# Kernel optimization log

Hardware: AMD Instinct MI355X
Metric: run time of the kernel (lower is better)

The kernel has to match this reference:

```python
import jax, jax.numpy as jnp
import numpy as np

DIM = 1024
HEADS = 16
N_SENTS = 64
N_ENTS = 16
BATCH = 32


def setup_inputs() -> dict:
    key = jax.random.key(0)
    ks = jax.random.split(key, 16)
    S, E, B, D = N_SENTS, N_ENTS, BATCH, DIM
    sc = 1.0 / np.sqrt(D)
    f32 = jnp.float32
    return {
        "entities": jax.random.normal(ks[0], (S * E, B, D), f32),
        "padding_mask": jnp.zeros((S * E, B), bool),
        "n_sents": S,
        # learned aggregation query, init uniform(-1, 1) as in the module
        "query": jax.random.uniform(ks[1], (1, 1, D), f32, -1.0, 1.0),
        # do_proj key/val Linear layers (torch Linear convention: y = x @ W.T + b)
        "Wk_lin": jax.random.normal(ks[2], (D, D), f32) * sc,
        "bk_lin": jnp.zeros((D,), f32),
        "Wv_lin": jax.random.normal(ks[3], (D, D), f32) * sc,
        "bv_lin": jnp.zeros((D,), f32),
        # MultiheadAttention in-projection (split q/k/v) and out-projection
        "Wq_in": jax.random.normal(ks[4], (D, D), f32) * sc,
        "bq_in": jnp.zeros((D,), f32),
        "Wk_in": jax.random.normal(ks[5], (D, D), f32) * sc,
        "bk_in": jnp.zeros((D,), f32),
        "Wv_in": jax.random.normal(ks[6], (D, D), f32) * sc,
        "bv_in": jnp.zeros((D,), f32),
        "Wo": jax.random.normal(ks[7], (D, D), f32) * sc,
        "bo": jnp.zeros((D,), f32),
    }


def reference(entities, padding_mask, n_sents, query,
              Wk_lin, bk_lin, Wv_lin, bv_lin,
              Wq_in, bq_in, Wk_in, bk_in, Wv_in, bv_in, Wo, bo):
    SE, B, D = entities.shape
    E = SE // n_sents
    H = HEADS
    hd = D // H

    # do_proj key/value linears
    keys = entities @ Wk_lin.T + bk_lin   # [SE, B, D]
    vals = entities @ Wv_lin.T + bv_lin   # [SE, B, D]

    # MHA in-projections. Query is a single learned vector shared across
    # sentences and batch, so project once: [H, hd], pre-scaled by 1/sqrt(hd).
    q = ((query[0, 0] @ Wq_in.T + bq_in).reshape(H, hd)) * (1.0 / np.sqrt(hd))
    # Honor the block-diagonal mask: query s only sees its n_ents key slice,
    # so reshape keys/vals to [S, E, B, H, hd] and never build [S, S*E] scores.
    k = (keys @ Wk_in.T + bk_in).reshape(n_sents, E, B, H, hd)
    v = (vals @ Wv_in.T + bv_in).reshape(n_sents, E, B, H, hd)

    scores = jnp.einsum('hd,sebhd->sbhe', q, k)            # [S, B, H, E]
    pm = padding_mask.reshape(n_sents, E, B).transpose(0, 2, 1)  # [S, B, E]
    scores = jnp.where(pm[:, :, None, :], -jnp.inf, scores)
    attn = jax.nn.softmax(scores, axis=-1)                 # [S, B, H, E]
    ctx = jnp.einsum('sbhe,sebhd->sbhd', attn, v).reshape(n_sents, B, D)
    return ctx @ Wo.T + bo                                  # [S, B, D]
```

## Files before the change

### kernel.cpp

```cpp
#include <hip/hip_runtime.h>
#include <hip/hip_bf16.h>

constexpr int kD  = 1024;
constexpr int kH  = 16;
constexpr int kHD = 64;
constexpr int kS  = 64;
constexpr int kE  = 16;
constexpr int kB  = 32;
constexpr int kSB = kS * kB;

typedef __attribute__((ext_vector_type(8))) short bfvec8;
typedef __attribute__((ext_vector_type(4))) float fvec4;

struct __align__(8)  bf4  { __hip_bfloat16 v[4]; };
struct __align__(16) bf8v { __hip_bfloat16 v[8]; };


__global__ __launch_bounds__(256) void k_pre(const float* __restrict__ Wq_in,
                                             const float* __restrict__ query,
                                             const float* __restrict__ bq_in,
                                             const float* __restrict__ Wv_in,
                                             const float* __restrict__ bv_lin,
                                             const float* __restrict__ bv_in,
                                             float* __restrict__ qs,
                                             float* __restrict__ cb,
                                             float* __restrict__ cvec) {
  int j = blockIdx.x, t = threadIdx.x;
  if (j == 0 && t < 16) cvec[t] = 0.f;
  const float *W, *vec, *bias;
  float scale;
  float* outp;
  int row;
  if (j < 1024) { W = Wq_in; vec = query;  bias = bq_in; scale = 0.125f; outp = qs; row = j; }
  else          { W = Wv_in; vec = bv_lin; bias = bv_in; scale = 1.0f;   outp = cb; row = j - 1024; }
  const float4* w4 = (const float4*)(W + (size_t)row * kD);
  const float4* v4 = (const float4*)vec;
  float4 a = w4[t], b = v4[t];
  float acc = a.x * b.x + a.y * b.y + a.z * b.z + a.w * b.w;
  #pragma unroll
  for (int o = 32; o >= 1; o >>= 1) acc += __shfl_xor(acc, o);
  __shared__ float red[4];
  if ((t & 63) == 0) red[t >> 6] = acc;
  __syncthreads();
  if (t == 0) outp[row] = (red[0] + red[1] + red[2] + red[3] + bias[row]) * scale;
}

__global__ __launch_bounds__(256) void k_w2(const float* __restrict__ qs,
                                            const float* __restrict__ Wk_in,
                                            const float* __restrict__ bk_lin,
                                            const float* __restrict__ bk_in,
                                            float* __restrict__ wmat,
                                            float* __restrict__ cvec) {
  int tid = blockIdx.x * 256 + threadIdx.x;
  int h = tid >> 10, d = tid & (kD - 1);
  float acc = 0.f;
  #pragma unroll 8
  for (int j = 0; j < kHD; j++)
    acc = fmaf(qs[h * kHD + j], Wk_in[(size_t)(h * kHD + j) * kD + d], acc);
  wmat[(size_t)h * kD + d] = acc;
  float val = acc * bk_lin[d];
  if (d < kHD) val += qs[h * kHD + d] * bk_in[h * kHD + d];
  #pragma unroll
  for (int o = 32; o >= 1; o >>= 1) val += __shfl_xor(val, o);
  if ((threadIdx.x & 63) == 0) atomicAdd(&cvec[h], val);
}

__global__ __launch_bounds__(256) void k_cvt(const float* __restrict__ in,
                                             __hip_bfloat16* __restrict__ out) {
  int i = (blockIdx.x * 256 + threadIdx.x) * 4;
  float4 v = *(const float4*)(in + i);
  bf4 o;
  o.v[0] = __float2bfloat16(v.x); o.v[1] = __float2bfloat16(v.y);
  o.v[2] = __float2bfloat16(v.z); o.v[3] = __float2bfloat16(v.w);
  *(bf4*)(out + i) = o;
}


__global__ __launch_bounds__(256) void k_attn_eagg(const float* __restrict__ ent,
                                                   const unsigned char* __restrict__ pmask,
                                                   const __hip_bfloat16* __restrict__ Ubf,
                                                   const float* __restrict__ cvec,
                                                   __hip_bfloat16* __restrict__ eagg) {
  __shared__ __hip_bfloat16 ent_s[kE][kD + 8];
  __shared__ float sred[4][kE][kH + 1];
  __shared__ __hip_bfloat16 attn_b[kH][32];
  int sb = blockIdx.x;
  int s = sb >> 5, b = sb & 31;
  int t = threadIdx.x, l = t & 63, w = t >> 6;
  int quad = l >> 4, lane16 = l & 15;

  const float* src = ent + (size_t)(s * kE) * kB * kD + (size_t)b * kD;
  #pragma unroll
  for (int it = 0; it < 8; it++) {
    int i = t + it * 256;
    int e = i >> 7, f = (i & 127) * 8;
    const float4* pp = (const float4*)(src + (size_t)e * kB * kD + f);
    float4 v0 = pp[0], v1 = pp[1];
    bf8v pk;
    pk.v[0] = __float2bfloat16(v0.x); pk.v[1] = __float2bfloat16(v0.y);
    pk.v[2] = __float2bfloat16(v0.z); pk.v[3] = __float2bfloat16(v0.w);
    pk.v[4] = __float2bfloat16(v1.x); pk.v[5] = __float2bfloat16(v1.y);
    pk.v[6] = __float2bfloat16(v1.z); pk.v[7] = __float2bfloat16(v1.w);
    *(bf8v*)&ent_s[e][f] = pk;
  }
  __syncthreads();

  fvec4 sacc = {};
  #pragma unroll
  for (int ks = 0; ks < 8; ks++) {
    int k0 = w * 256 + ks * 32 + quad * 8;
    bfvec8 a = *(const bfvec8*)&ent_s[lane16][k0];
    bfvec8 bb = *(const bfvec8*)&Ubf[(size_t)lane16 * kD + k0];
    sacc = __builtin_amdgcn_mfma_f32_16x16x32_bf16(a, bb, sacc, 0, 0, 0);
  }
  #pragma unroll
  for (int i = 0; i < 4; i++) sred[w][quad * 4 + i][lane16] = sacc[i];
  __syncthreads();

  {
    int h = t >> 4, e = t & 15;
    float sc = sred[0][e][h] + sred[1][e][h] + sred[2][e][h] + sred[3][e][h] + cvec[h];
    if (pmask[(size_t)(s * kE + e) * kB + b]) sc = -INFINITY;
    float m = sc;
    #pragma unroll
    for (int o = 8; o >= 1; o >>= 1) m = fmaxf(m, __shfl_xor(m, o, 16));
    float ex = __expf(sc - m);
    float sum = ex;
    #pragma unroll
    for (int o = 8; o >= 1; o >>= 1) sum += __shfl_xor(sum, o, 16);
    attn_b[h][e] = __float2bfloat16(ex / sum);
    attn_b[h][e + 16] = __float2bfloat16(0.f);
  }
  __syncthreads();

  bfvec8 bfrag = *(const bfvec8*)&attn_b[lane16][quad * 8];
  __hip_bfloat16* dst = eagg + (size_t)sb * (kH * kD);
  for (int tt = 0; tt < 16; tt++) {
    int dme = (w * 16 + tt) * 16 + lane16;
    bfvec8 afrag = {};
    if (quad < 2) {
      #pragma unroll
      for (int j = 0; j < 8; j++)
        afrag[j] = *(const short*)&ent_s[quad * 8 + j][dme];
    }
    fvec4 acc = {};
    acc = __builtin_amdgcn_mfma_f32_16x16x32_bf16(afrag, bfrag, acc, 0, 0, 0);
    int d0 = (w * 16 + tt) * 16 + quad * 4;
    bf4 o;
    o.v[0] = __float2bfloat16(acc[0]); o.v[1] = __float2bfloat16(acc[1]);
    o.v[2] = __float2bfloat16(acc[2]); o.v[3] = __float2bfloat16(acc[3]);
    *(bf4*)&dst[(size_t)lane16 * kD + d0] = o;
  }
}


__device__ __forceinline__ void stage_row(const __hip_bfloat16* g, __hip_bfloat16* s) {
  *(bf8v*)s = *(const bf8v*)g;
}
__device__ __forceinline__ void stage_row(const float* g, __hip_bfloat16* s) {
  const float4* p = (const float4*)g;
  float4 v0 = p[0], v1 = p[1];
  bf8v pk;
  pk.v[0] = __float2bfloat16(v0.x); pk.v[1] = __float2bfloat16(v0.y);
  pk.v[2] = __float2bfloat16(v0.z); pk.v[3] = __float2bfloat16(v0.w);
  pk.v[4] = __float2bfloat16(v1.x); pk.v[5] = __float2bfloat16(v1.y);
  pk.v[6] = __float2bfloat16(v1.z); pk.v[7] = __float2bfloat16(v1.w);
  *(bf8v*)s = pk;
}


template <int MODE, typename TA, typename TB, typename TC>
__global__ __launch_bounds__(256) void k_gemm_mfma(
    const TA* __restrict__ Abase, int lda, long aBatch,
    const TB* __restrict__ Bbase, int ldb, long bBatch,
    TC* __restrict__ Cbase, int ldc, long cBatch,
    const float* __restrict__ bias, long biasBatch, int Ksz) {
  const TA* Ag = Abase + (size_t)blockIdx.z * aBatch;
  const TB* Bg = Bbase + (size_t)blockIdx.z * bBatch;
  TC* Cg = Cbase + (size_t)blockIdx.z * cBatch;
  const float* biasp = bias ? bias + (size_t)blockIdx.z * biasBatch : nullptr;
  const int m0 = blockIdx.x * 64, n0 = blockIdx.y * 64;
  __shared__ __hip_bfloat16 As[64][72];
  __shared__ __hip_bfloat16 Bs[64][72];
  const int t = threadIdx.x;
  const int l = t & 63, w = t >> 6;
  const int quad = l >> 4, col = l & 15;
  fvec4 acc[4] = {};
  for (int k0 = 0; k0 < Ksz; k0 += 64) {
    #pragma unroll
    for (int c = t; c < 512; c += 256) {
      int row = c >> 3, kq = (c & 7) * 8;
      stage_row(Ag + (size_t)(m0 + row) * lda + k0 + kq, &As[row][kq]);
      stage_row(Bg + (size_t)(n0 + row) * ldb + k0 + kq, &Bs[row][kq]);
    }
    __syncthreads();
    #pragma unroll
    for (int ks = 0; ks < 64; ks += 32) {
      bfvec8 a = *(const bfvec8*)&As[w * 16 + col][ks + quad * 8];
      #pragma unroll
      for (int nt = 0; nt < 4; nt++) {
        bfvec8 b = *(const bfvec8*)&Bs[nt * 16 + col][ks + quad * 8];
        acc[nt] = __builtin_amdgcn_mfma_f32_16x16x32_bf16(a, b, acc[nt], 0, 0, 0);
      }
    }
    __syncthreads();
  }
  #pragma unroll
  for (int nt = 0; nt < 4; nt++) {
    int n = n0 + nt * 16 + col;
    float bv = biasp ? biasp[n] : 0.f;
    #pragma unroll
    for (int i = 0; i < 4; i++) {
      int r = m0 + w * 16 + quad * 4 + i;
      float v = acc[nt][i] + bv;
      if constexpr (MODE == 0) ((float*)Cg)[(size_t)r * ldc + n] = v;
      else ((__hip_bfloat16*)Cg)[(size_t)r * ldc + n] = __float2bfloat16(v);
    }
  }
}


__global__ __launch_bounds__(256) void k_gemm_nn(
    const float* __restrict__ Ag, int lda,
    const float* __restrict__ Bg, int ldb,
    __hip_bfloat16* __restrict__ Cg, int ldc, int Ksz) {
  const int m0 = blockIdx.x * 64, n0 = blockIdx.y * 64;
  __shared__ __hip_bfloat16 As[64][72];
  __shared__ __hip_bfloat16 Bs[64][72];
  const int t = threadIdx.x;
  const int l = t & 63, w = t >> 6;
  const int quad = l >> 4, col = l & 15;
  fvec4 acc[4] = {};
  for (int k0 = 0; k0 < Ksz; k0 += 64) {
    #pragma unroll
    for (int c = t; c < 512; c += 256) {
      int row = c >> 3, kq = (c & 7) * 8;
      stage_row(Ag + (size_t)(m0 + row) * lda + k0 + kq, &As[row][kq]);
      const float4* pb = (const float4*)(Bg + (size_t)(k0 + row) * ldb + n0 + kq);
      float4 b0 = pb[0], b1 = pb[1];
      Bs[kq + 0][row] = __float2bfloat16(b0.x);
      Bs[kq + 1][row] = __float2bfloat16(b0.y);
      Bs[kq + 2][row] = __float2bfloat16(b0.z);
      Bs[kq + 3][row] = __float2bfloat16(b0.w);
      Bs[kq + 4][row] = __float2bfloat16(b1.x);
      Bs[kq + 5][row] = __float2bfloat16(b1.y);
      Bs[kq + 6][row] = __float2bfloat16(b1.z);
      Bs[kq + 7][row] = __float2bfloat16(b1.w);
    }
    __syncthreads();
    #pragma unroll
    for (int ks = 0; ks < 64; ks += 32) {
      bfvec8 a = *(const bfvec8*)&As[w * 16 + col][ks + quad * 8];
      #pragma unroll
      for (int nt = 0; nt < 4; nt++) {
        bfvec8 b = *(const bfvec8*)&Bs[nt * 16 + col][ks + quad * 8];
        acc[nt] = __builtin_amdgcn_mfma_f32_16x16x32_bf16(a, b, acc[nt], 0, 0, 0);
      }
    }
    __syncthreads();
  }
  #pragma unroll
  for (int nt = 0; nt < 4; nt++) {
    int n = n0 + nt * 16 + col;
    #pragma unroll
    for (int i = 0; i < 4; i++) {
      int r = m0 + w * 16 + quad * 4 + i;
      Cg[(size_t)r * ldc + n] = __float2bfloat16(acc[nt][i]);
    }
  }
}

extern "C" void kernel_launch(void* const* d_in, const int* in_sizes, int n_in,
                              void* d_out, int out_size, void* d_ws, size_t ws_size,
                              hipStream_t stream) {
  const float* ent            = (const float*)d_in[0];
  const unsigned char* pmask  = (const unsigned char*)d_in[1];
  const float* query          = (const float*)d_in[3];
  const float* Wk_lin         = (const float*)d_in[4];
  const float* bk_lin         = (const float*)d_in[5];
  const float* Wv_lin         = (const float*)d_in[6];
  const float* bv_lin         = (const float*)d_in[7];
  const float* Wq_in          = (const float*)d_in[8];
  const float* bq_in          = (const float*)d_in[9];
  const float* Wk_in          = (const float*)d_in[10];
  const float* bk_in          = (const float*)d_in[11];
  const float* Wv_in          = (const float*)d_in[12];
  const float* bv_in          = (const float*)d_in[13];
  const float* Wo             = (const float*)d_in[14];
  const float* bo             = (const float*)d_in[15];
  float* out = (float*)d_out;

  float* p = (float*)d_ws;
  float* qs   = p; p += 1024;
  float* wmat = p; p += 64 * kD;
  float* cvec = p; p += 256;
  float* cb   = p; p += kD;
  __hip_bfloat16* bp = (__hip_bfloat16*)p;
  __hip_bfloat16* Ubf  = bp; bp += (size_t)64 * kD;
  __hip_bfloat16* Mmat = bp; bp += (size_t)kD * kD;
  __hip_bfloat16* Wobf = bp; bp += (size_t)kD * kD;
  __hip_bfloat16* ctx2 = bp; bp += (size_t)kSB * kD;
  __hip_bfloat16* eagg = bp;

  k_pre<<<2048, 256, 0, stream>>>(Wq_in, query, bq_in, Wv_in, bv_lin, bv_in, qs, cb, cvec);
  k_w2<<<64, 256, 0, stream>>>(qs, Wk_in, bk_lin, bk_in, wmat, cvec);
  k_cvt<<<1024, 256, 0, stream>>>(Wo, Wobf);
  k_gemm_nn<<<dim3(1, 16, 1), 256, 0, stream>>>(wmat, kD, Wk_lin, kD, Ubf, kD, kD);
  k_gemm_nn<<<dim3(16, 16, 1), 256, 0, stream>>>(Wv_in, kD, Wv_lin, kD, Mmat, kD, kD);

  k_attn_eagg<<<kSB, 256, 0, stream>>>(ent, pmask, Ubf, cvec, eagg);
  k_gemm_mfma<2><<<dim3(kSB / 64, 1, kH), 256, 0, stream>>>(
      eagg, kH * kD, (long)kD, Mmat, kD, (long)(kHD * kD),
      ctx2, kD, (long)kHD, cb, (long)kHD, kD);
  k_gemm_mfma<0><<<dim3(kSB / 64, kD / 64, 1), 256, 0, stream>>>(
      ctx2, kD, 0L, Wobf, kD, 0L, out, kD, 0L, bo, 0L, kD);
}
```

Baseline: 354.7 us.

## Double-buffer GEMMs, swizzle workgroups, merge precompute kernels, halve attention MFMA waste

Adds register-prefetch double buffering and workgroup-ID swizzling to both MFMA GEMM kernels, removing one barrier per K step. Folds the Wo conversion and the Wk bias projection into k_pre. It now computes Wk_in·Wk_lin as a full batched GEMM alongside Wv_in·Wv_lin, then forms U from that product in a new small kernel. The attention aggregation kernel uses a cross-lane shuffle so each MFMA carries useful data in both halves rather than zero padding. Together these cut launch count and stall time, but the extra full 1024x1024 GEMM adds precompute work and the product is rounded to bf16 before U is formed.

```diff
diff --git a/kernel.cpp b/kernel.cpp
--- a/kernel.cpp
+++ b/kernel.cpp
@@ -11,10 +11,10 @@
 
 typedef __attribute__((ext_vector_type(8))) short bfvec8;
 typedef __attribute__((ext_vector_type(4))) float fvec4;
+typedef __attribute__((ext_vector_type(4))) int   ivec4;
 
 struct __align__(8)  bf4  { __hip_bfloat16 v[4]; };
 struct __align__(16) bf8v { __hip_bfloat16 v[8]; };
-
 
 __global__ __launch_bounds__(256) void k_pre(const float* __restrict__ Wq_in,
                                              const float* __restrict__ query,
@@ -22,17 +22,31 @@
                                              const float* __restrict__ Wv_in,
                                              const float* __restrict__ bv_lin,
                                              const float* __restrict__ bv_in,
+                                             const float* __restrict__ Wk_in,
+                                             const float* __restrict__ bk_lin,
+                                             const float* __restrict__ bk_in,
+                                             const float* __restrict__ Wo,
                                              float* __restrict__ qs,
                                              float* __restrict__ cb,
-                                             float* __restrict__ cvec) {
+                                             float* __restrict__ kb2,
+                                             __hip_bfloat16* __restrict__ Wobf) {
   int j = blockIdx.x, t = threadIdx.x;
-  if (j == 0 && t < 16) cvec[t] = 0.f;
+  if (j >= 3072) {
+    int i = (j - 3072) * kD + t * 4;
+    float4 v = *(const float4*)(Wo + i);
+    bf4 o;
+    o.v[0] = __float2bfloat16(v.x); o.v[1] = __float2bfloat16(v.y);
+    o.v[2] = __float2bfloat16(v.z); o.v[3] = __float2bfloat16(v.w);
+    *(bf4*)(Wobf + i) = o;
+    return;
+  }
   const float *W, *vec, *bias;
   float scale;
   float* outp;
   int row;
-  if (j < 1024) { W = Wq_in; vec = query;  bias = bq_in; scale = 0.125f; outp = qs; row = j; }
-  else          { W = Wv_in; vec = bv_lin; bias = bv_in; scale = 1.0f;   outp = cb; row = j - 1024; }
+  if (j < 1024)      { W = Wq_in; vec = query;  bias = bq_in; scale = 0.125f; outp = qs;  row = j; }
+  else if (j < 2048) { W = Wv_in; vec = bv_lin; bias = bv_in; scale = 1.0f;   outp = cb;  row = j - 1024; }
+  else               { W = Wk_in; vec = bk_lin; bias = bk_in; scale = 1.0f;   outp = kb2; row = j - 2048; }
   const float4* w4 = (const float4*)(W + (size_t)row * kD);
   const float4* v4 = (const float4*)vec;
   float4 a = w4[t], b = v4[t];
@@ -45,36 +59,35 @@
   if (t == 0) outp[row] = (red[0] + red[1] + red[2] + red[3] + bias[row]) * scale;
 }
 
-__global__ __launch_bounds__(256) void k_w2(const float* __restrict__ qs,
-                                            const float* __restrict__ Wk_in,
-                                            const float* __restrict__ bk_lin,
-                                            const float* __restrict__ bk_in,
-                                            float* __restrict__ wmat,
-                                            float* __restrict__ cvec) {
-  int tid = blockIdx.x * 256 + threadIdx.x;
-  int h = tid >> 10, d = tid & (kD - 1);
+__global__ __launch_bounds__(256) void k_w2p(const float* __restrict__ qs,
+                                             const __hip_bfloat16* __restrict__ KK,
+                                             const float* __restrict__ kb2,
+                                             __hip_bfloat16* __restrict__ Ubf,
+                                             float* __restrict__ cvec) {
+  int bq = blockIdx.x;
+  int h = bq >> 2;
+  int n = (bq & 3) * 256 + threadIdx.x;
   float acc = 0.f;
   #pragma unroll 8
   for (int j = 0; j < kHD; j++)
-    acc = fmaf(qs[h * kHD + j], Wk_in[(size_t)(h * kHD + j) * kD + d], acc);
-  wmat[(size_t)h * kD + d] = acc;
-  float val = acc * bk_lin[d];
-  if (d < kHD) val += qs[h * kHD + d] * bk_in[h * kHD + d];
-  #pragma unroll
-  for (int o = 32; o >= 1; o >>= 1) val += __shfl_xor(val, o);
-  if ((threadIdx.x & 63) == 0) atomicAdd(&cvec[h], val);
-}
-
-__global__ __launch_bounds__(256) void k_cvt(const float* __restrict__ in,
-                                             __hip_bfloat16* __restrict__ out) {
-  int i = (blockIdx.x * 256 + threadIdx.x) * 4;
-  float4 v = *(const float4*)(in + i);
+    acc = fmaf(qs[h * kHD + j], __bfloat162float(KK[(size_t)(h * kHD + j) * kD + n]), acc);
+  Ubf[(size_t)h * kD + n] = __float2bfloat16(acc);
+  if ((bq & 3) == 0 && threadIdx.x < 64) {
+    int t = threadIdx.x;
+    float v = qs[h * kHD + t] * kb2[h * kHD + t];
+    #pragma unroll
+    for (int o = 32; o >= 1; o >>= 1) v += __shfl_xor(v, o);
+    if (t == 0) cvec[h] = v;
+  }
+}
+
+
+__device__ __forceinline__ void st4(__hip_bfloat16* dst, fvec4 a) {
   bf4 o;
-  o.v[0] = __float2bfloat16(v.x); o.v[1] = __float2bfloat16(v.y);
-  o.v[2] = __float2bfloat16(v.z); o.v[3] = __float2bfloat16(v.w);
-  *(bf4*)(out + i) = o;
-}
-
+  o.v[0] = __float2bfloat16(a[0]); o.v[1] = __float2bfloat16(a[1]);
+  o.v[2] = __float2bfloat16(a[2]); o.v[3] = __float2bfloat16(a[3]);
+  *(bf4*)dst = o;
+}
 
 __global__ __launch_bounds__(256) void k_attn_eagg(const float* __restrict__ ent,
                                                    const unsigned char* __restrict__ pmask,
@@ -135,31 +148,31 @@
 
   bfvec8 bfrag = *(const bfvec8*)&attn_b[lane16][quad * 8];
   __hip_bfloat16* dst = eagg + (size_t)sb * (kH * kD);
-  for (int tt = 0; tt < 16; tt++) {
-    int dme = (w * 16 + tt) * 16 + lane16;
-    bfvec8 afrag = {};
-    if (quad < 2) {
-      #pragma unroll
-      for (int j = 0; j < 8; j++)
-        afrag[j] = *(const short*)&ent_s[quad * 8 + j][dme];
-    }
-    fvec4 acc = {};
-    acc = __builtin_amdgcn_mfma_f32_16x16x32_bf16(afrag, bfrag, acc, 0, 0, 0);
-    int d0 = (w * 16 + tt) * 16 + quad * 4;
-    bf4 o;
-    o.v[0] = __float2bfloat16(acc[0]); o.v[1] = __float2bfloat16(acc[1]);
-    o.v[2] = __float2bfloat16(acc[2]); o.v[3] = __float2bfloat16(acc[3]);
-    *(bf4*)&dst[(size_t)lane16 * kD + d0] = o;
-  }
-}
-
-
-__device__ __forceinline__ void stage_row(const __hip_bfloat16* g, __hip_bfloat16* s) {
-  *(bf8v*)s = *(const bf8v*)g;
-}
-__device__ __forceinline__ void stage_row(const float* g, __hip_bfloat16* s) {
-  const float4* p = (const float4*)g;
-  float4 v0 = p[0], v1 = p[1];
+  int eq = (quad & 1) * 8;
+  #pragma unroll
+  for (int tp = 0; tp < 8; tp++) {
+    int tSel = (quad < 2) ? tp : (tp + 8);
+    int dme = (w * 16 + tSel) * 16 + lane16;
+    bfvec8 val;
+    #pragma unroll
+    for (int j = 0; j < 8; j++)
+      val[j] = *(const short*)&ent_s[eq + j][dme];
+    ivec4 vi = __builtin_bit_cast(ivec4, val);
+    ivec4 wi;
+    #pragma unroll
+    for (int r = 0; r < 4; r++) wi[r] = __shfl_xor(vi[r], 32);
+    bfvec8 valB = __builtin_bit_cast(bfvec8, wi);
+    fvec4 aA = {}, aB = {};
+    aA = __builtin_amdgcn_mfma_f32_16x16x32_bf16(val,  bfrag, aA, 0, 0, 0);
+    aB = __builtin_amdgcn_mfma_f32_16x16x32_bf16(valB, bfrag, aB, 0, 0, 0);
+    int d0A = (w * 16 + tp) * 16 + quad * 4;
+    int d0B = (w * 16 + tp + 8) * 16 + quad * 4;
+    st4(&dst[(size_t)lane16 * kD + d0A], aA);
+    st4(&dst[(size_t)lane16 * kD + d0B], aB);
+  }
+}
+
+__device__ __forceinline__ void cvt8(__hip_bfloat16* s, float4 v0, float4 v1) {
   bf8v pk;
   pk.v[0] = __float2bfloat16(v0.x); pk.v[1] = __float2bfloat16(v0.y);
   pk.v[2] = __float2bfloat16(v0.z); pk.v[3] = __float2bfloat16(v0.w);
@@ -169,41 +182,62 @@
 }
 
 
-template <int MODE, typename TA, typename TB, typename TC>
+template <int MODE, typename TC>
 __global__ __launch_bounds__(256) void k_gemm_mfma(
-    const TA* __restrict__ Abase, int lda, long aBatch,
-    const TB* __restrict__ Bbase, int ldb, long bBatch,
+    const __hip_bfloat16* __restrict__ Abase, int lda, long aBatch,
+    const __hip_bfloat16* __restrict__ Bbase, int ldb, long bBatch,
     TC* __restrict__ Cbase, int ldc, long cBatch,
     const float* __restrict__ bias, long biasBatch, int Ksz) {
-  const TA* Ag = Abase + (size_t)blockIdx.z * aBatch;
-  const TB* Bg = Bbase + (size_t)blockIdx.z * bBatch;
-  TC* Cg = Cbase + (size_t)blockIdx.z * cBatch;
-  const float* biasp = bias ? bias + (size_t)blockIdx.z * biasBatch : nullptr;
-  const int m0 = blockIdx.x * 64, n0 = blockIdx.y * 64;
-  __shared__ __hip_bfloat16 As[64][72];
-  __shared__ __hip_bfloat16 Bs[64][72];
+  int nwg = gridDim.x * gridDim.y * gridDim.z;
+  int wgid = blockIdx.x + gridDim.x * (blockIdx.y + gridDim.y * blockIdx.z);
+  int per = nwg >> 3;
+  int swz = (wgid & 7) * per + (wgid >> 3);
+  int bx = swz % gridDim.x;
+  int rr = swz / gridDim.x;
+  int by = rr % gridDim.y;
+  int bz = rr / gridDim.y;
+  const __hip_bfloat16* Ag = Abase + (size_t)bz * aBatch;
+  const __hip_bfloat16* Bg = Bbase + (size_t)bz * bBatch;
+  TC* Cg = Cbase + (size_t)bz * cBatch;
+  const float* biasp = bias ? bias + (size_t)bz * biasBatch : nullptr;
+  const int m0 = bx * 64, n0 = by * 64;
+  __shared__ __hip_bfloat16 As[2][64][72];
+  __shared__ __hip_bfloat16 Bs[2][64][72];
   const int t = threadIdx.x;
   const int l = t & 63, w = t >> 6;
   const int quad = l >> 4, col = l & 15;
+  const int row0 = t >> 3, kq = (t & 7) * 8;
   fvec4 acc[4] = {};
+  bf8v ra0, ra1, rb0, rb1;
+  auto LDT = [&](int k0) {
+    ra0 = *(const bf8v*)(Ag + (size_t)(m0 + row0) * lda + k0 + kq);
+    ra1 = *(const bf8v*)(Ag + (size_t)(m0 + row0 + 32) * lda + k0 + kq);
+    rb0 = *(const bf8v*)(Bg + (size_t)(n0 + row0) * ldb + k0 + kq);
+    rb1 = *(const bf8v*)(Bg + (size_t)(n0 + row0 + 32) * ldb + k0 + kq);
+  };
+  auto STT = [&](int buf) {
+    *(bf8v*)&As[buf][row0][kq] = ra0;
+    *(bf8v*)&As[buf][row0 + 32][kq] = ra1;
+    *(bf8v*)&Bs[buf][row0][kq] = rb0;
+    *(bf8v*)&Bs[buf][row0 + 32][kq] = rb1;
+  };
+  LDT(0); STT(0);
+  int cur = 0;
   for (int k0 = 0; k0 < Ksz; k0 += 64) {
-    #pragma unroll
-    for (int c = t; c < 512; c += 256) {
-      int row = c >> 3, kq = (c & 7) * 8;
-      stage_row(Ag + (size_t)(m0 + row) * lda + k0 + kq, &As[row][kq]);
-      stage_row(Bg + (size_t)(n0 + row) * ldb + k0 + kq, &Bs[row][kq]);
-    }
+    bool more = (k0 + 64) < Ksz;
+    if (more) LDT(k0 + 64);
     __syncthreads();
     #pragma unroll
     for (int ks = 0; ks < 64; ks += 32) {
-      bfvec8 a = *(const bfvec8*)&As[w * 16 + col][ks + quad * 8];
+      bfvec8 a = *(const bfvec8*)&As[cur][w * 16 + col][ks + quad * 8];
       #pragma unroll
       for (int nt = 0; nt < 4; nt++) {
-        bfvec8 b = *(const bfvec8*)&Bs[nt * 16 + col][ks + quad * 8];
+        bfvec8 b = *(const bfvec8*)&Bs[cur][nt * 16 + col][ks + quad * 8];
         acc[nt] = __builtin_amdgcn_mfma_f32_16x16x32_bf16(a, b, acc[nt], 0, 0, 0);
       }
     }
-    __syncthreads();
+    if (more) STT(cur ^ 1);
+    cur ^= 1;
   }
   #pragma unroll
   for (int nt = 0; nt < 4; nt++) {
@@ -221,43 +255,76 @@
 
 
 __global__ __launch_bounds__(256) void k_gemm_nn(
-    const float* __restrict__ Ag, int lda,
-    const float* __restrict__ Bg, int ldb,
-    __hip_bfloat16* __restrict__ Cg, int ldc, int Ksz) {
-  const int m0 = blockIdx.x * 64, n0 = blockIdx.y * 64;
-  __shared__ __hip_bfloat16 As[64][72];
-  __shared__ __hip_bfloat16 Bs[64][72];
+    const float* __restrict__ A0, const float* __restrict__ B0,
+    const float* __restrict__ A1, const float* __restrict__ B1,
+    __hip_bfloat16* __restrict__ C0, __hip_bfloat16* __restrict__ C1, int Ksz) {
+  int nwg = gridDim.x * gridDim.y * gridDim.z;
+  int wgid = blockIdx.x + gridDim.x * (blockIdx.y + gridDim.y * blockIdx.z);
+  int per = nwg >> 3;
+  int swz = (wgid & 7) * per + (wgid >> 3);
+  int bx = swz % gridDim.x;
+  int rr = swz / gridDim.x;
+  int by = rr % gridDim.y;
+  int bz = rr / gridDim.y;
+  const float* Ag = bz ? A1 : A0;
+  const float* Bg = bz ? B1 : B0;
+  __hip_bfloat16* Cg = bz ? C1 : C0;
+  const int m0 = bx * 64, n0 = by * 64;
+  __shared__ __hip_bfloat16 As[2][64][72];
+  __shared__ __hip_bfloat16 Bs[2][64][72];
   const int t = threadIdx.x;
   const int l = t & 63, w = t >> 6;
   const int quad = l >> 4, col = l & 15;
+  const int row0 = t >> 3, kq = (t & 7) * 8;
   fvec4 acc[4] = {};
+  float4 a00, a01, a10, a11, b00, b01, b10, b11;
+  auto LDT = [&](int k0) {
+    const float4* p0 = (const float4*)(Ag + (size_t)(m0 + row0) * kD + k0 + kq);
+    a00 = p0[0]; a01 = p0[1];
+    const float4* p1 = (const float4*)(Ag + (size_t)(m0 + row0 + 32) * kD + k0 + kq);
+    a10 = p1[0]; a11 = p1[1];
+    const float4* q0 = (const float4*)(Bg + (size_t)(k0 + row0) * kD + n0 + kq);
+    b00 = q0[0]; b01 = q0[1];
+    const float4* q1 = (const float4*)(Bg + (size_t)(k0 + row0 + 32) * kD + n0 + kq);
+    b10 = q1[0]; b11 = q1[1];
+  };
+  auto STT = [&](int buf) {
+    cvt8(&As[buf][row0][kq], a00, a01);
+    cvt8(&As[buf][row0 + 32][kq], a10, a11);
+    Bs[buf][kq + 0][row0] = __float2bfloat16(b00.x);
+    Bs[buf][kq + 1][row0] = __float2bfloat16(b00.y);
+    Bs[buf][kq + 2][row0] = __float2bfloat16(b00.z);
+    Bs[buf][kq + 3][row0] = __float2bfloat16(b00.w);
+    Bs[buf][kq + 4][row0] = __float2bfloat16(b01.x);
+    Bs[buf][kq + 5][row0] = __float2bfloat16(b01.y);
+    Bs[buf][kq + 6][row0] = __float2bfloat16(b01.z);
+    Bs[buf][kq + 7][row0] = __float2bfloat16(b01.w);
+    Bs[buf][kq + 0][row0 + 32] = __float2bfloat16(b10.x);
+    Bs[buf][kq + 1][row0 + 32] = __float2bfloat16(b10.y);
+    Bs[buf][kq + 2][row0 + 32] = __float2bfloat16(b10.z);
+    Bs[buf][kq + 3][row0 + 32] = __float2bfloat16(b10.w);
+    Bs[buf][kq + 4][row0 + 32] = __float2bfloat16(b11.x);
+    Bs[buf][kq + 5][row0 + 32] = __float2bfloat16(b11.y);
+    Bs[buf][kq + 6][row0 + 32] = __float2bfloat16(b11.z);
+    Bs[buf][kq + 7][row0 + 32] = __float2bfloat16(b11.w);
+  };
+  LDT(0); STT(0);
+  int cur = 0;
   for (int k0 = 0; k0 < Ksz; k0 += 64) {
-    #pragma unroll
-    for (int c = t; c < 512; c += 256) {
-      int row = c >> 3, kq = (c & 7) * 8;
-      stage_row(Ag + (size_t)(m0 + row) * lda + k0 + kq, &As[row][kq]);
-      const float4* pb = (const float4*)(Bg + (size_t)(k0 + row) * ldb + n0 + kq);
-      float4 b0 = pb[0], b1 = pb[1];
-      Bs[kq + 0][row] = __float2bfloat16(b0.x);
-      Bs[kq + 1][row] = __float2bfloat16(b0.y);
-      Bs[kq + 2][row] = __float2bfloat16(b0.z);
-      Bs[kq + 3][row] = __float2bfloat16(b0.w);
-      Bs[kq + 4][row] = __float2bfloat16(b1.x);
-      Bs[kq + 5][row] = __float2bfloat16(b1.y);
-      Bs[kq + 6][row] = __float2bfloat16(b1.z);
-      Bs[kq + 7][row] = __float2bfloat16(b1.w);
-    }
+    bool more = (k0 + 64) < Ksz;
+    if (more) LDT(k0 + 64);
     __syncthreads();
     #pragma unroll
     for (int ks = 0; ks < 64; ks += 32) {
-      bfvec8 a = *(const bfvec8*)&As[w * 16 + col][ks + quad * 8];
+      bfvec8 a = *(const bfvec8*)&As[cur][w * 16 + col][ks + quad * 8];
       #pragma unroll
       for (int nt = 0; nt < 4; nt++) {
-        bfvec8 b = *(const bfvec8*)&Bs[nt * 16 + col][ks + quad * 8];
+        bfvec8 b = *(const bfvec8*)&Bs[cur][nt * 16 + col][ks + quad * 8];
         acc[nt] = __builtin_amdgcn_mfma_f32_16x16x32_bf16(a, b, acc[nt], 0, 0, 0);
       }
     }
-    __syncthreads();
+    if (more) STT(cur ^ 1);
+    cur ^= 1;
   }
   #pragma unroll
   for (int nt = 0; nt < 4; nt++) {
@@ -265,7 +332,7 @@
     #pragma unroll
     for (int i = 0; i < 4; i++) {
       int r = m0 + w * 16 + quad * 4 + i;
-      Cg[(size_t)r * ldc + n] = __float2bfloat16(acc[nt][i]);
+      Cg[(size_t)r * kD + n] = __float2bfloat16(acc[nt][i]);
     }
   }
 }
@@ -292,26 +359,27 @@
 
   float* p = (float*)d_ws;
   float* qs   = p; p += 1024;
-  float* wmat = p; p += 64 * kD;
   float* cvec = p; p += 256;
   float* cb   = p; p += kD;
+  float* kb2  = p; p += kD;
   __hip_bfloat16* bp = (__hip_bfloat16*)p;
-  __hip_bfloat16* Ubf  = bp; bp += (size_t)64 * kD;
+  __hip_bfloat16* Ubf  = bp; bp += (size_t)kH * kD;
   __hip_bfloat16* Mmat = bp; bp += (size_t)kD * kD;
+  __hip_bfloat16* KKbf = bp; bp += (size_t)kD * kD;
   __hip_bfloat16* Wobf = bp; bp += (size_t)kD * kD;
   __hip_bfloat16* ctx2 = bp; bp += (size_t)kSB * kD;
   __hip_bfloat16* eagg = bp;
 
-  k_pre<<<2048, 256, 0, stream>>>(Wq_in, query, bq_in, Wv_in, bv_lin, bv_in, qs, cb, cvec);
-  k_w2<<<64, 256, 0, stream>>>(qs, Wk_in, bk_lin, bk_in, wmat, cvec);
-  k_cvt<<<1024, 256, 0, stream>>>(Wo, Wobf);
-  k_gemm_nn<<<dim3(1, 16, 1), 256, 0, stream>>>(wmat, kD, Wk_lin, kD, Ubf, kD, kD);
-  k_gemm_nn<<<dim3(16, 16, 1), 256, 0, stream>>>(Wv_in, kD, Wv_lin, kD, Mmat, kD, kD);
+  k_pre<<<4096, 256, 0, stream>>>(Wq_in, query, bq_in, Wv_in, bv_lin, bv_in,
+                                  Wk_in, bk_lin, bk_in, Wo, qs, cb, kb2, Wobf);
+  k_gemm_nn<<<dim3(16, 16, 2), 256, 0, stream>>>(Wv_in, Wv_lin, Wk_in, Wk_lin,
+                                                 Mmat, KKbf, kD);
+  k_w2p<<<64, 256, 0, stream>>>(qs, KKbf, kb2, Ubf, cvec);
 
   k_attn_eagg<<<kSB, 256, 0, stream>>>(ent, pmask, Ubf, cvec, eagg);
-  k_gemm_mfma<2><<<dim3(kSB / 64, 1, kH), 256, 0, stream>>>(
+  k_gemm_mfma<2, __hip_bfloat16><<<dim3(kSB / 64, 1, kH), 256, 0, stream>>>(
       eagg, kH * kD, (long)kD, Mmat, kD, (long)(kHD * kD),
       ctx2, kD, (long)kHD, cb, (long)kHD, kD);
-  k_gemm_mfma<0><<<dim3(kSB / 64, kD / 64, 1), 256, 0, stream>>>(
+  k_gemm_mfma<0, float><<<dim3(kSB / 64, kD / 64, 1), 256, 0, stream>>>(
       ctx2, kD, 0L, Wobf, kD, 0L, out, kD, 0L, bo, 0L, kD);
 }
```

New measurement: 390.1 us. 1.1x slower.
